# Kernel optimization log

Hardware: AMD Instinct MI355X
Metric: run time of the kernel (lower is better)

The kernel has to match this reference:

```python
import jax, jax.numpy as jnp
import numpy as np

N_NODES = 50000
N_EDGES = 1600000
IN_C = 256
HID_C = 128
OUT_C = 16
HEADS = 8
NEG_SLOPE = 0.2  # PyG GATConv default


def gat_layer(x, src, dst, W, att_src, att_dst, bias, heads, out_c):
    """PyG-style GATConv (eval mode, add_self_loops already applied to src/dst).
    x: [N, F_in], W: [F_in, heads*out_c], att_*: [heads, out_c], bias: [heads*out_c].
    Returns concatenated heads: [N, heads*out_c]."""
    N = x.shape[0]
    h = (x @ W).reshape(N, heads, out_c)                  # [N, H, C]
    a_src = (h * att_src[None]).sum(-1)                   # [N, H]
    a_dst = (h * att_dst[None]).sum(-1)                   # [N, H]
    alpha = a_src[src] + a_dst[dst]                       # [E, H]
    alpha = jax.nn.leaky_relu(alpha, NEG_SLOPE)
    # segment softmax over incoming edges of each destination node
    amax = jax.ops.segment_max(alpha, dst, num_segments=N)  # [N, H]
    alpha = jnp.exp(alpha - jax.lax.stop_gradient(amax)[dst])
    denom = jax.ops.segment_sum(alpha, dst, num_segments=N)  # [N, H]
    w = alpha / denom[dst]                                # [E, H]
    msg = h[src] * w[:, :, None]                          # [E, H, C]
    out = jax.ops.segment_sum(msg, dst, num_segments=N)   # [N, H, C]
    return out.reshape(N, heads * out_c) + bias


def setup_inputs() -> dict:
    key = jax.random.key(0)
    ks = jax.random.split(key, 10)
    x = jax.random.normal(ks[0], (N_NODES, IN_C), dtype=jnp.float32)
    edge_index = jax.random.randint(ks[1], (2, N_EDGES), 0, N_NODES, dtype=jnp.int32)
    c1 = HID_C // HEADS  # 16 per head
    s1 = 1.0 / np.sqrt(IN_C)
    s2 = 1.0 / np.sqrt(HID_C)
    return {
        "x": x,
        "edge_index": edge_index,
        "W1": jax.random.normal(ks[2], (IN_C, HEADS * c1), dtype=jnp.float32) * s1,
        "att_src1": jax.random.normal(ks[3], (HEADS, c1), dtype=jnp.float32) * s1,
        "att_dst1": jax.random.normal(ks[4], (HEADS, c1), dtype=jnp.float32) * s1,
        "bias1": jnp.zeros((HEADS * c1,), dtype=jnp.float32),
        "W2": jax.random.normal(ks[5], (HID_C, OUT_C), dtype=jnp.float32) * s2,
        "att_src2": jax.random.normal(ks[6], (1, OUT_C), dtype=jnp.float32) * s2,
        "att_dst2": jax.random.normal(ks[7], (1, OUT_C), dtype=jnp.float32) * s2,
        "bias2": jnp.zeros((OUT_C,), dtype=jnp.float32),
    }


def reference(x, edge_index, W1, att_src1, att_dst1, bias1, W2, att_src2, att_dst2, bias2):
    N = x.shape[0]
    loop = jnp.arange(N, dtype=edge_index.dtype)
    src = jnp.concatenate([edge_index[0], loop])  # add_self_loops=True (PyG default)
    dst = jnp.concatenate([edge_index[1], loop])
    h = gat_layer(x, src, dst, W1, att_src1, att_dst1, bias1, HEADS, HID_C // HEADS)
    h = jax.nn.relu(h)
    # F.dropout with training=False is identity (eval mode)
    out = gat_layer(h, src, dst, W2, att_src2, att_dst2, bias2, 1, OUT_C)
    return out
```

## Files before the change

kernel.cpp:

```cpp
#include <hip/hip_runtime.h>
#include <hip/hip_bf16.h>


#define NN 50000
#define NE 1600000
#define NBK 196
#define NB_SC 512
#define CHUNK (NE / NB_SC)
#define NCH (NB_SC * 4)
#define GB1 782
#define GB2 1563

typedef __attribute__((ext_vector_type(8))) short bf16x8;
typedef __attribute__((ext_vector_type(4))) float f32x4;

__device__ __forceinline__ float lrelu(float x) { return fmaxf(x, 0.2f * x); }

__device__ __forceinline__ float ldf(const void* p, int i, int isbf) {
  return isbf ? __bfloat162float(((const __hip_bfloat16*)p)[i])
              : ((const float*)p)[i];
}
__device__ __forceinline__ short f2bf_bits(float v) {
  __hip_bfloat16 h = __float2bfloat16(v);
  return *reinterpret_cast<short*>(&h);
}
__device__ __forceinline__ float bfs2f(short b) {
  unsigned int u = ((unsigned int)(unsigned short)b) << 16;
  union { unsigned int u; float f; } c; c.u = u; return c.f;
}
__device__ __forceinline__ unsigned short f2h_bits(float v) {
  _Float16 h = (_Float16)v;
  return *reinterpret_cast<unsigned short*>(&h);
}
__device__ __forceinline__ float h2f(unsigned short b) {
  _Float16 h = *reinterpret_cast<_Float16*>(&b);
  return (float)h;
}

#define OFF_H1   ((size_t)0)
#define OFF_H    ((size_t)25600000)
#define OFF_H2   ((size_t)51200000)
#define OFF_AS1  ((size_t)54400000)
#define OFF_AD1  ((size_t)56000000)
#define OFF_AS2  ((size_t)57600000)
#define OFF_AD2  ((size_t)57800000)
#define OFF_CNT  ((size_t)58000000)
#define OFF_OFFS ((size_t)58400000)
#define OFF_CSR  ((size_t)58600000)
#define OFF_WP1  ((size_t)65000000)
#define OFF_BCNT ((size_t)65065536)
#define OFF_BBASE ((size_t)65066560)
#define OFF_FLAG ((size_t)65068608)

__global__ void detect_dtype(const unsigned int* __restrict__ x, int* __restrict__ flag) {
  __shared__ int s[256];
  int t = threadIdx.x;
  unsigned int w = x[t * 97 + 5];
  unsigned int e = (w >> 7) & 0xFF;
  s[t] = (e >= 116 && e <= 138) ? 1 : 0;
  __syncthreads();
  for (int off = 128; off > 0; off >>= 1) {
    if (t < off) s[t] += s[t + off];
    __syncthreads();
  }
  if (t == 0) *flag = (s[0] >= 128) ? 1 : 0;
}

__global__ void repack_w1(const void* __restrict__ W1, short* __restrict__ Wp,
                          const int* __restrict__ flag) {
  int i = blockIdx.x * 256 + threadIdx.x;
  if (i >= 256 * 128) return;
  int f = *flag;
  int j = i & 7, q = (i >> 3) & 3, c = (i >> 5) & 127, t = i >> 12;
  int src = (t * 32 + q * 8 + j) * 128 + c;
  Wp[i] = f ? ((const short*)W1)[src] : f2bf_bits(((const float*)W1)[src]);
}

__global__ __launch_bounds__(256) void fat1(const void* __restrict__ X,
                                            const short* __restrict__ Wp,
                                            short* __restrict__ H1b,
                                            const int* __restrict__ flag,
                                            const int* __restrict__ dst,
                                            int* __restrict__ HB) {
  __shared__ int h[4][224];
  if (blockIdx.x < GB1) {
    int wave = threadIdx.x >> 6, lane = threadIdx.x & 63;
    int rowbase = blockIdx.x * 64 + wave * 16;
    int l15 = lane & 15, quad = lane >> 4;
    int f = *flag;
    int arow = rowbase + l15;
    if (arow >= NN) arow = NN - 1;
    f32x4 acc[8];
#pragma unroll
    for (int ct = 0; ct < 8; ++ct) acc[ct] = (f32x4){0.f, 0.f, 0.f, 0.f};
    size_t abase = (size_t)arow * 256 + quad * 8;
#pragma unroll
    for (int kt = 0; kt < 8; ++kt) {
      bf16x8 a;
      if (f) {
        a = *(const bf16x8*)((const short*)X + abase + kt * 32);
      } else {
        const float* xp = (const float*)X + abase + kt * 32;
        float4 v0 = *(const float4*)xp, v1 = *(const float4*)(xp + 4);
        a[0] = f2bf_bits(v0.x); a[1] = f2bf_bits(v0.y);
        a[2] = f2bf_bits(v0.z); a[3] = f2bf_bits(v0.w);
        a[4] = f2bf_bits(v1.x); a[5] = f2bf_bits(v1.y);
        a[6] = f2bf_bits(v1.z); a[7] = f2bf_bits(v1.w);
      }
#pragma unroll
      for (int ct = 0; ct < 8; ++ct) {
        bf16x8 b = *(const bf16x8*)(Wp + ((kt * 128 + ct * 16 + l15) * 4 + quad) * 8);
        acc[ct] = __builtin_amdgcn_mfma_f32_16x16x32_bf16(a, b, acc[ct], 0, 0, 0);
      }
    }
    int r0 = rowbase + quad * 4;
#pragma unroll
    for (int ct = 0; ct < 8; ++ct)
#pragma unroll
      for (int r = 0; r < 4; ++r) {
        int row = r0 + r;
        if (row < NN) H1b[(size_t)row * 128 + ct * 16 + l15] = f2bf_bits(acc[ct][r]);
      }
  } else {
    int b = blockIdx.x - GB1;
    int t = threadIdx.x, w = t >> 6;
    for (int i = t; i < 4 * 224; i += 256) (&h[0][0])[i] = 0;
    __syncthreads();
    int e0 = b * CHUNK, e1 = e0 + CHUNK;
    for (int e = e0 + t; e < e1; e += 256) atomicAdd(&h[w][dst[e] >> 8], 1);
    __syncthreads();
    int chunk0 = b * 4;
    for (int i = t; i < 4 * NBK; i += 256) {
      int ww = i / NBK, k = i - ww * NBK;
      HB[(chunk0 + ww) * NBK + k] = h[ww][k];
    }
  }
}

__global__ __launch_bounds__(256) void fat2(const short* __restrict__ H1b,
                                            const void* __restrict__ as1,
                                            const void* __restrict__ ad1,
                                            float* __restrict__ AS,
                                            float* __restrict__ AD,
                                            const int* __restrict__ flag,
                                            int* __restrict__ HB,
                                            int* __restrict__ total) {
  __shared__ float s_as[128], s_ad[128];
  __shared__ int ts[256];
  int t = threadIdx.x;
  if (blockIdx.x < GB2) {
    int f = *flag;
    if (t < 128) { s_as[t] = ldf(as1, t, f); s_ad[t] = ldf(ad1, t, f); }
    __syncthreads();
    int tid = blockIdx.x * 256 + t;
    if (tid >= NN * 8) return;
    int n = tid >> 3, hh = tid & 7;
    const bf16x8* hp = (const bf16x8*)(H1b + (size_t)n * 128 + hh * 16);
    bf16x8 v0 = hp[0], v1 = hp[1];
    float as = 0.f, ad = 0.f;
#pragma unroll
    for (int i = 0; i < 8; ++i) {
      int b = hh * 16 + i;
      float x0 = bfs2f(v0[i]), x1 = bfs2f(v1[i]);
      as += x0 * s_as[b] + x1 * s_as[b + 8];
      ad += x0 * s_ad[b] + x1 * s_ad[b + 8];
    }
    AS[tid] = as; AD[tid] = ad;
  } else {
    int k = blockIdx.x - GB2;
    int base = t * 8;
    int v[8]; int s = 0;
#pragma unroll
    for (int i = 0; i < 8; ++i) { v[i] = HB[(base + i) * NBK + k]; s += v[i]; }
    ts[t] = s;
    __syncthreads();
    for (int off = 1; off < 256; off <<= 1) {
      int a = (t >= off) ? ts[t - off] : 0;
      __syncthreads();
      ts[t] += a;
      __syncthreads();
    }
    int ex = ts[t] - s;
#pragma unroll
    for (int i = 0; i < 8; ++i) { HB[(base + i) * NBK + k] = ex; ex += v[i]; }
    if (t == 255) total[k] = ts[255];
  }
}

__global__ void scat_scan2(const int* __restrict__ total, int* __restrict__ bbase,
                           int* __restrict__ bcnt) {
  __shared__ int sd[256];
  int t = threadIdx.x;
  int v = (t < NBK) ? total[t] : 0;
  sd[t] = v;
  __syncthreads();
  for (int off = 1; off < 256; off <<= 1) {
    int a = (t >= off) ? sd[t - off] : 0;
    __syncthreads();
    sd[t] += a;
    __syncthreads();
  }
  if (t < NBK) { bbase[t] = sd[t] - v; bcnt[t] = v; }
}

__global__ __launch_bounds__(256) void scat_write(const int* __restrict__ src,
                                                  const int* __restrict__ dst,
                                                  const int* __restrict__ HB,
                                                  const int* __restrict__ bbase,
                                                  unsigned int* __restrict__ EPp) {
  __shared__ int sc[4][224];
  int t = threadIdx.x, w = t >> 6, lane = t & 63;
  int chunk = blockIdx.x * 4 + w;
  for (int k = lane; k < NBK; k += 64)
    sc[w][k] = bbase[k] + HB[chunk * NBK + k];
  __syncthreads();
  int e0 = blockIdx.x * CHUNK, e1 = e0 + CHUNK;
  for (int e = e0 + t; e < e1; e += 256) {
    int d = dst[e];
    int p = atomicAdd(&sc[w][d >> 8], 1);
    EPp[p] = ((unsigned int)(d & 255) << 16) | (unsigned int)src[e];
  }
}

__global__ __launch_bounds__(1024) void bucket_csr(const unsigned int* __restrict__ EPp,
                                                   const int* __restrict__ bcnt,
                                                   const int* __restrict__ bbase,
                                                   int* __restrict__ cnt,
                                                   int* __restrict__ offs,
                                                   unsigned short* __restrict__ csr) {
  __shared__ int h[256], sc[256], lc[256];
  int b = blockIdx.x, t = threadIdx.x;
  int gbase = bbase[b], n = bcnt[b];
  if (t < 256) h[t] = 0;
  __syncthreads();
  for (int i = t; i < n; i += 1024) atomicAdd(&h[(EPp[gbase + i] >> 16) & 255], 1);
  __syncthreads();
  int v = 0;
  if (t < 256) { v = h[t]; sc[t] = v; }
  __syncthreads();
  for (int off = 1; off < 256; off <<= 1) {
    int add = (t >= off && t < 256) ? sc[t - off] : 0;
    __syncthreads();
    if (t < 256) sc[t] += add;
    __syncthreads();
  }
  if (t < 256) {
    int ex = sc[t] - v;
    int node = (b << 8) + t;
    if (node < NN) { cnt[node] = v; offs[node] = gbase + ex; }
    lc[t] = ex;
  }
  __syncthreads();
  for (int i = t; i < n; i += 1024) {
    unsigned int p = EPp[gbase + i];
    int pos = atomicAdd(&lc[(p >> 16) & 255], 1);
    csr[gbase + pos] = (unsigned short)(p & 0xFFFF);
  }
}

__global__ __launch_bounds__(256) void agg1(const short* __restrict__ H1b,
                                            const float* __restrict__ AS,
                                            const float* __restrict__ AD,
                                            const int* __restrict__ offs,
                                            const int* __restrict__ cnt,
                                            const unsigned short* __restrict__ csr,
                                            const void* __restrict__ bias1,
                                            short* __restrict__ Hb,
                                            const int* __restrict__ flag) {
  int lane = threadIdx.x & 63;
  int node = blockIdx.x * 4 + (threadIdx.x >> 6);
  int f = *flag;
  int start = offs[node], deg = cnt[node];
  int g = lane >> 3, k = lane & 7;
  float adst = AD[node * 8 + k];
  float acc[16];
#pragma unroll
  for (int i = 0; i < 16; ++i) acc[i] = 0.f;
  float dsum = 0.f;
  if (g == 0) {
    float p = __expf(lrelu(AS[node * 8 + k] + adst));
    dsum = p;
    const bf16x8* hp = (const bf16x8*)(H1b + (size_t)node * 128 + k * 16);
    bf16x8 v0 = hp[0], v1 = hp[1];
#pragma unroll
    for (int i = 0; i < 8; ++i) {
      acc[i] = p * bfs2f(v0[i]);
      acc[8 + i] = p * bfs2f(v1[i]);
    }
  }
  int s = (g < deg) ? (int)csr[start + g] : -1;
  float a_c = 0.f; bf16x8 v0, v1;
  if (s >= 0) {
    a_c = AS[s * 8 + k];
    const bf16x8* hp = (const bf16x8*)(H1b + (size_t)s * 128 + k * 16);
    v0 = hp[0]; v1 = hp[1];
  }
  for (int eb = 0; eb < deg; eb += 8) {
    int en = eb + 8 + g;
    int sn = (en < deg) ? (int)csr[start + en] : -1;
    float a_n = 0.f; bf16x8 w0, w1;
    if (sn >= 0) {
      a_n = AS[sn * 8 + k];
      const bf16x8* hp = (const bf16x8*)(H1b + (size_t)sn * 128 + k * 16);
      w0 = hp[0]; w1 = hp[1];
    }
    if (s >= 0) {
      float p = __expf(lrelu(a_c + adst));
      dsum += p;
#pragma unroll
      for (int i = 0; i < 8; ++i) {
        acc[i] += p * bfs2f(v0[i]);
        acc[8 + i] += p * bfs2f(v1[i]);
      }
    }
    s = sn; a_c = a_n; v0 = w0; v1 = w1;
  }
#pragma unroll
  for (int i = 0; i < 16; ++i) {
    acc[i] += __shfl_xor(acc[i], 8);
    acc[i] += __shfl_xor(acc[i], 16);
    acc[i] += __shfl_xor(acc[i], 32);
  }
  dsum += __shfl_xor(dsum, 8);
  dsum += __shfl_xor(dsum, 16);
  dsum += __shfl_xor(dsum, 32);
  if (g == 0) {
    float inv = 1.0f / dsum;
    int c0 = k * 16;
    bf16x8 o0, o1;
#pragma unroll
    for (int i = 0; i < 8; ++i) {
      o0[i] = f2bf_bits(fmaxf(acc[i] * inv + ldf(bias1, c0 + i, f), 0.f));
      o1[i] = f2bf_bits(fmaxf(acc[8 + i] * inv + ldf(bias1, c0 + 8 + i, f), 0.f));
    }
    *(bf16x8*)(Hb + (size_t)node * 128 + c0) = o0;
    *(bf16x8*)(Hb + (size_t)node * 128 + c0 + 8) = o1;
  }
}

__global__ __launch_bounds__(256) void gemm2_a2(const short* __restrict__ Hb,
                                                const void* __restrict__ W2,
                                                const void* __restrict__ as2,
                                                const void* __restrict__ ad2,
                                                unsigned short* __restrict__ H2h,
                                                float* __restrict__ AS2,
                                                float* __restrict__ AD2,
                                                const int* __restrict__ flag) {
  __shared__ float sW[2048];
  __shared__ float s_as[16], s_ad[16];
  int t = threadIdx.x;
  int f = *flag;
  for (int i = t; i < 2048; i += 256) sW[i] = ldf(W2, i, f);
  if (t < 16) { s_as[t] = ldf(as2, t, f); s_ad[t] = ldf(ad2, t, f); }
  __syncthreads();
  int n = blockIdx.x * 16 + (t >> 4), c = t & 15;
  const bf16x8* hp = (const bf16x8*)(Hb + (size_t)n * 128);
  float acc = 0.f;
#pragma unroll 4
  for (int k8 = 0; k8 < 16; ++k8) {
    bf16x8 v = hp[k8];
#pragma unroll
    for (int i = 0; i < 8; ++i) acc += bfs2f(v[i]) * sW[(k8 * 8 + i) * 16 + c];
  }
  H2h[n * 16 + c] = f2h_bits(acc);
  float vs = acc * s_as[c], vd = acc * s_ad[c];
#pragma unroll
  for (int off = 1; off < 16; off <<= 1) {
    vs += __shfl_xor(vs, off);
    vd += __shfl_xor(vd, off);
  }
  if (c == 0) { AS2[n] = vs; AD2[n] = vd; }
}

__global__ __launch_bounds__(256) void agg2(const unsigned short* __restrict__ H2h,
                                            const float* __restrict__ AS2,
                                            const float* __restrict__ AD2,
                                            const int* __restrict__ offs,
                                            const int* __restrict__ cnt,
                                            const unsigned short* __restrict__ csr,
                                            const void* __restrict__ bias2,
                                            void* __restrict__ outv,
                                            const int* __restrict__ flag) {
  int lane = threadIdx.x & 63;
  int node = blockIdx.x * 4 + (threadIdx.x >> 6);
  int f = *flag;
  int start = offs[node], deg = cnt[node];
  int g = lane >> 3, k = lane & 7;
  float adst = AD2[node];
  float a0 = 0.f, a1 = 0.f, dsum = 0.f;
  if (g == 0) {
    float p = __expf(lrelu(AS2[node] + adst));
    dsum = p;
    unsigned int hv = *(const unsigned int*)(H2h + (size_t)node * 16 + k * 2);
    a0 = p * h2f((unsigned short)(hv & 0xFFFF));
    a1 = p * h2f((unsigned short)(hv >> 16));
  }
  int s = (g < deg) ? (int)csr[start + g] : -1;
  float as_c = 0.f; unsigned int hv_c = 0;
  if (s >= 0) {
    as_c = AS2[s];
    hv_c = *(const unsigned int*)(H2h + (size_t)s * 16 + k * 2);
  }
  for (int eb = 0; eb < deg; eb += 8) {
    int en = eb + 8 + g;
    int sn = (en < deg) ? (int)csr[start + en] : -1;
    float as_n = 0.f; unsigned int hv_n = 0;
    if (sn >= 0) {
      as_n = AS2[sn];
      hv_n = *(const unsigned int*)(H2h + (size_t)sn * 16 + k * 2);
    }
    if (s >= 0) {
      float p = __expf(lrelu(as_c + adst));
      dsum += p;
      a0 += p * h2f((unsigned short)(hv_c & 0xFFFF));
      a1 += p * h2f((unsigned short)(hv_c >> 16));
    }
    s = sn; as_c = as_n; hv_c = hv_n;
  }
  a0 += __shfl_xor(a0, 8);  a0 += __shfl_xor(a0, 16);  a0 += __shfl_xor(a0, 32);
  a1 += __shfl_xor(a1, 8);  a1 += __shfl_xor(a1, 16);  a1 += __shfl_xor(a1, 32);
  dsum += __shfl_xor(dsum, 8); dsum += __shfl_xor(dsum, 16); dsum += __shfl_xor(dsum, 32);
  if (g == 0) {
    float inv = 1.0f / dsum;
    float o0 = a0 * inv + ldf(bias2, k * 2 + 0, f);
    float o1 = a1 * inv + ldf(bias2, k * 2 + 1, f);
    size_t base = (size_t)node * 16 + k * 2;
    if (f) {
      ((__hip_bfloat16*)outv)[base] = __float2bfloat16(o0);
      ((__hip_bfloat16*)outv)[base + 1] = __float2bfloat16(o1);
    } else {
      *(float2*)((float*)outv + base) = make_float2(o0, o1);
    }
  }
}

extern "C" void kernel_launch(void* const* d_in, const int* in_sizes, int n_in,
                              void* d_out, int out_size, void* d_ws, size_t ws_size,
                              hipStream_t stream) {
  const void* x = d_in[0];
  const int* ei = (const int*)d_in[1];
  const void* W1 = d_in[2];
  const void* as1 = d_in[3];
  const void* ad1 = d_in[4];
  const void* b1 = d_in[5];
  const void* W2 = d_in[6];
  const void* as2 = d_in[7];
  const void* ad2 = d_in[8];
  const void* b2 = d_in[9];
  char* ws = (char*)d_ws;

  short* H1b = (short*)(ws + OFF_H1);
  short* Hb = (short*)(ws + OFF_H);
  unsigned int* EPp = (unsigned int*)(ws + OFF_H);
  unsigned short* H2h = (unsigned short*)(ws + OFF_H2);
  int* HB = (int*)(ws + OFF_H2);
  float* AS1 = (float*)(ws + OFF_AS1);
  float* AD1 = (float*)(ws + OFF_AD1);
  float* AS2 = (float*)(ws + OFF_AS2);
  float* AD2 = (float*)(ws + OFF_AD2);
  int* CNT = (int*)(ws + OFF_CNT);
  int* OFFS = (int*)(ws + OFF_OFFS);
  unsigned short* CSR = (unsigned short*)(ws + OFF_CSR);
  short* Wp = (short*)(ws + OFF_WP1);
  int* BCNT = (int*)(ws + OFF_BCNT);
  int* BBASE = (int*)(ws + OFF_BBASE);
  int* FLAG = (int*)(ws + OFF_FLAG);

  detect_dtype<<<1, 256, 0, stream>>>((const unsigned int*)x, FLAG);
  repack_w1<<<128, 256, 0, stream>>>(W1, Wp, FLAG);
  fat1<<<GB1 + NB_SC, 256, 0, stream>>>(x, Wp, H1b, FLAG, ei + NE, HB);
  fat2<<<GB2 + NBK, 256, 0, stream>>>(H1b, as1, ad1, AS1, AD1, FLAG, HB, BCNT);
  scat_scan2<<<1, 256, 0, stream>>>(BCNT, BBASE, BCNT);
  scat_write<<<NB_SC, 256, 0, stream>>>(ei, ei + NE, HB, BBASE, EPp);
  bucket_csr<<<NBK, 1024, 0, stream>>>(EPp, BCNT, BBASE, CNT, OFFS, CSR);

  agg1<<<NN / 4, 256, 0, stream>>>(H1b, AS1, AD1, OFFS, CNT, CSR, b1, Hb, FLAG);
  gemm2_a2<<<NN / 16, 256, 0, stream>>>(Hb, W2, as2, ad2, H2h, AS2, AD2, FLAG);
  agg2<<<NN / 4, 256, 0, stream>>>(H2h, AS2, AD2, OFFS, CNT, CSR, b2, d_out, FLAG);
}
```

Before: 275.3 us.

## Stage bucket scatter in LDS per block and merge dtype detection into repack

The scatter pass now builds a per-block local histogram and prefix scan, writes the packed edges into a shared-memory staging buffer grouped by bucket, and then copies each bucket's run to global memory as contiguous writes instead of scattering random 4-byte stores. The per-wave histogram granularity is reduced to per-block, which shrinks the HB array and the column scan in fat2. Dtype detection is folded into repack_w1, so every block recomputes the flag and one kernel launch disappears. In exchange, scat_write re-reads dst, uses about 12.5KB of LDS for staging, and loops serially over 196 buckets during the copy-out.

```diff
diff --git a/kernel.cpp b/kernel.cpp
--- a/kernel.cpp
+++ b/kernel.cpp
@@ -7,7 +7,6 @@
 #define NBK 196
 #define NB_SC 512
 #define CHUNK (NE / NB_SC)
-#define NCH (NB_SC * 4)
 #define GB1 782
 #define GB2 1563
 
@@ -52,10 +51,12 @@
 #define OFF_BBASE ((size_t)65066560)
 #define OFF_FLAG ((size_t)65068608)
 
-__global__ void detect_dtype(const unsigned int* __restrict__ x, int* __restrict__ flag) {
+__global__ void repack_w1(const void* __restrict__ W1, short* __restrict__ Wp,
+                          const unsigned int* __restrict__ xw, int* __restrict__ flag) {
   __shared__ int s[256];
+  __shared__ int sf;
   int t = threadIdx.x;
-  unsigned int w = x[t * 97 + 5];
+  unsigned int w = xw[t * 97 + 5];
   unsigned int e = (w >> 7) & 0xFF;
   s[t] = (e >= 116 && e <= 138) ? 1 : 0;
   __syncthreads();
@@ -63,16 +64,15 @@
     if (t < off) s[t] += s[t + off];
     __syncthreads();
   }
-  if (t == 0) *flag = (s[0] >= 128) ? 1 : 0;
-}
-
-__global__ void repack_w1(const void* __restrict__ W1, short* __restrict__ Wp,
-                          const int* __restrict__ flag) {
-  int i = blockIdx.x * 256 + threadIdx.x;
-  if (i >= 256 * 128) return;
-  int f = *flag;
-  int j = i & 7, q = (i >> 3) & 3, c = (i >> 5) & 127, t = i >> 12;
-  int src = (t * 32 + q * 8 + j) * 128 + c;
+  if (t == 0) {
+    sf = (s[0] >= 128) ? 1 : 0;
+    if (blockIdx.x == 0) *flag = sf;
+  }
+  __syncthreads();
+  int f = sf;
+  int i = blockIdx.x * 256 + t;
+  int j = i & 7, q = (i >> 3) & 3, c = (i >> 5) & 127, tt = i >> 12;
+  int src = (tt * 32 + q * 8 + j) * 128 + c;
   Wp[i] = f ? ((const short*)W1)[src] : f2bf_bits(((const float*)W1)[src]);
 }
 
@@ -82,7 +82,7 @@
                                             const int* __restrict__ flag,
                                             const int* __restrict__ dst,
                                             int* __restrict__ HB) {
-  __shared__ int h[4][224];
+  __shared__ int h[224];
   if (blockIdx.x < GB1) {
     int wave = threadIdx.x >> 6, lane = threadIdx.x & 63;
     int rowbase = blockIdx.x * 64 + wave * 16;
@@ -123,17 +123,13 @@
       }
   } else {
     int b = blockIdx.x - GB1;
-    int t = threadIdx.x, w = t >> 6;
-    for (int i = t; i < 4 * 224; i += 256) (&h[0][0])[i] = 0;
+    int t = threadIdx.x;
+    for (int i = t; i < 224; i += 256) h[i] = 0;
     __syncthreads();
     int e0 = b * CHUNK, e1 = e0 + CHUNK;
-    for (int e = e0 + t; e < e1; e += 256) atomicAdd(&h[w][dst[e] >> 8], 1);
-    __syncthreads();
-    int chunk0 = b * 4;
-    for (int i = t; i < 4 * NBK; i += 256) {
-      int ww = i / NBK, k = i - ww * NBK;
-      HB[(chunk0 + ww) * NBK + k] = h[ww][k];
-    }
+    for (int e = e0 + t; e < e1; e += 256) atomicAdd(&h[dst[e] >> 8], 1);
+    __syncthreads();
+    for (int i = t; i < NBK; i += 256) HB[b * NBK + i] = h[i];
   }
 }
 
@@ -168,10 +164,8 @@
     AS[tid] = as; AD[tid] = ad;
   } else {
     int k = blockIdx.x - GB2;
-    int base = t * 8;
-    int v[8]; int s = 0;
-#pragma unroll
-    for (int i = 0; i < 8; ++i) { v[i] = HB[(base + i) * NBK + k]; s += v[i]; }
+    int v0 = HB[(t * 2) * NBK + k], v1 = HB[(t * 2 + 1) * NBK + k];
+    int s = v0 + v1;
     ts[t] = s;
     __syncthreads();
     for (int off = 1; off < 256; off <<= 1) {
@@ -181,8 +175,8 @@
       __syncthreads();
     }
     int ex = ts[t] - s;
-#pragma unroll
-    for (int i = 0; i < 8; ++i) { HB[(base + i) * NBK + k] = ex; ex += v[i]; }
+    HB[(t * 2) * NBK + k] = ex;
+    HB[(t * 2 + 1) * NBK + k] = ex + v0;
     if (t == 255) total[k] = ts[255];
   }
 }
@@ -208,17 +202,40 @@
                                                   const int* __restrict__ HB,
                                                   const int* __restrict__ bbase,
                                                   unsigned int* __restrict__ EPp) {
-  __shared__ int sc[4][224];
-  int t = threadIdx.x, w = t >> 6, lane = t & 63;
-  int chunk = blockIdx.x * 4 + w;
-  for (int k = lane; k < NBK; k += 64)
-    sc[w][k] = bbase[k] + HB[chunk * NBK + k];
-  __syncthreads();
-  int e0 = blockIdx.x * CHUNK, e1 = e0 + CHUNK;
+  __shared__ int h[224], sc[256], lofs[224], lc[224], gd[224];
+  __shared__ unsigned int EB[CHUNK];
+  int t = threadIdx.x, b = blockIdx.x;
+  for (int i = t; i < 224; i += 256) h[i] = 0;
+  __syncthreads();
+  int e0 = b * CHUNK, e1 = e0 + CHUNK;
+  for (int e = e0 + t; e < e1; e += 256) atomicAdd(&h[dst[e] >> 8], 1);
+  __syncthreads();
+  int v = (t < NBK) ? h[t] : 0;
+  sc[t] = v;
+  __syncthreads();
+  for (int off = 1; off < 256; off <<= 1) {
+    int a = (t >= off) ? sc[t - off] : 0;
+    __syncthreads();
+    sc[t] += a;
+    __syncthreads();
+  }
+  if (t < NBK) {
+    int ex = sc[t] - v;
+    lofs[t] = ex; lc[t] = ex;
+    gd[t] = bbase[t] + HB[b * NBK + t];
+  }
+  __syncthreads();
   for (int e = e0 + t; e < e1; e += 256) {
     int d = dst[e];
-    int p = atomicAdd(&sc[w][d >> 8], 1);
-    EPp[p] = ((unsigned int)(d & 255) << 16) | (unsigned int)src[e];
+    int pos = atomicAdd(&lc[d >> 8], 1);
+    EB[pos] = ((unsigned int)(d & 255) << 16) | (unsigned int)src[e];
+  }
+  __syncthreads();
+  for (int k = 0; k < NBK; ++k) {
+    int len = h[k];
+    if (!len) continue;
+    int g0 = gd[k], l0 = lofs[k];
+    for (int i = t; i < len; i += 256) EPp[g0 + i] = EB[l0 + i];
   }
 }
 
@@ -466,8 +483,7 @@
   int* BBASE = (int*)(ws + OFF_BBASE);
   int* FLAG = (int*)(ws + OFF_FLAG);
 
-  detect_dtype<<<1, 256, 0, stream>>>((const unsigned int*)x, FLAG);
-  repack_w1<<<128, 256, 0, stream>>>(W1, Wp, FLAG);
+  repack_w1<<<128, 256, 0, stream>>>(W1, Wp, (const unsigned int*)x, FLAG);
   fat1<<<GB1 + NB_SC, 256, 0, stream>>>(x, Wp, H1b, FLAG, ei + NE, HB);
   fat2<<<GB2 + NBK, 256, 0, stream>>>(H1b, as1, ad1, AS1, AD1, FLAG, HB, BCNT);
   scat_scan2<<<1, 256, 0, stream>>>(BCNT, BBASE, BCNT);
```

Result: slower. 306.0 us (+11.2%).
